# Kernel optimization log

Measured on AMD Instinct MI355X. Metric: run time of the kernel, lower is better.

Reference implementation:

```python
import jax, jax.numpy as jnp
import numpy as np

COS_EPS = 1e-6
LN_EPS = 1e-5

def _cosine_sim(a, b):
    # PyTorch F.cosine_similarity(dim=1, eps): dot / (max(||a||,eps)*max(||b||,eps))
    dot = jnp.sum(a * b, axis=1)
    na = jnp.maximum(jnp.linalg.norm(a, axis=1), COS_EPS)
    nb = jnp.maximum(jnp.linalg.norm(b, axis=1), COS_EPS)
    return dot / (na * nb)

def _layer_norm(x, gamma, beta):
    mu = jnp.mean(x, axis=-1, keepdims=True)
    var = jnp.mean(jnp.square(x - mu), axis=-1, keepdims=True)
    return (x - mu) * jax.lax.rsqrt(var + LN_EPS) * gamma + beta

def setup_inputs() -> dict:
    B, I, H = 8192, 1024, 1024
    key = jax.random.key(0)
    ks = jax.random.split(key, 10)
    s_in = 1.0 / np.sqrt(I + H)
    s_im = 1.0 / np.sqrt(I)
    return {
        "x": jax.random.normal(ks[0], (B, I), jnp.float32),
        "hx": jax.random.normal(ks[1], (B, H), jnp.float32),
        "cx": jax.random.normal(ks[2], (B, H), jnp.float32),
        # main gate linear: [I+H, 4H]
        "W": jax.random.uniform(ks[3], (I + H, 4 * H), jnp.float32, -s_in, s_in),
        "b": jax.random.uniform(ks[4], (4 * H,), jnp.float32, -s_in, s_in),
        # input_mapped: [I, H]
        "Wm": jax.random.uniform(ks[5], (I, H), jnp.float32, -s_im, s_im),
        "bm": jax.random.uniform(ks[6], (H,), jnp.float32, -s_im, s_im),
        # 4 LayerNorms (i, f, g, o)
        "gammas": 1.0 + 0.1 * jax.random.normal(ks[7], (4, H), jnp.float32),
        "betas": 0.1 * jax.random.normal(ks[8], (4, H), jnp.float32),
    }

def reference(x, hx, cx, W, b, Wm, bm, gammas, betas):
    H = hx.shape[1]
    # cosine attention gate between mapped input and hidden state
    input_mapped = x @ Wm + bm                                   # [B, H]
    attn = jax.nn.sigmoid(_cosine_sim(input_mapped, hx))[:, None]  # [B, 1]
    x_mod = x + attn * x
    gates = jnp.concatenate([x_mod, hx], axis=1) @ W + b         # [B, 4H]
    i_g, f_g, g_g, o_g = jnp.split(gates, 4, axis=1)
    i_g = jax.nn.sigmoid(_layer_norm(i_g, gammas[0], betas[0]))
    f_g = jax.nn.sigmoid(_layer_norm(f_g, gammas[1], betas[1]))
    g_g = jnp.tanh(_layer_norm(g_g, gammas[2], betas[2]))
    o_g = jax.nn.sigmoid(_layer_norm(o_g, gammas[3], betas[3]))
    cx_new = f_g * cx + i_g * g_g
    hx_new = o_g * jnp.tanh(cx_new)
    gate_co = jax.nn.sigmoid((_cosine_sim(hx_new, cx_new)[:, None] + 1.0) / 2.0)
    hx_modulated = hx_new + hx_new * gate_co
    return (hx_modulated, cx_new)
```

## Files before the change

kernel.cpp:

```cpp
#include <hip/hip_runtime.h>
#include <hip/hip_bf16.h>

#define DEV __device__ __forceinline__

typedef unsigned short u16;
typedef unsigned int u32;
typedef __attribute__((ext_vector_type(8))) short bf16x8;
typedef __attribute__((ext_vector_type(4))) float f32x4;

DEV float bf2f(u16 v) { u32 u = ((u32)v) << 16; return __builtin_bit_cast(float, u); }
DEV u16 f2bf(float f) {
    u32 u = __builtin_bit_cast(u32, f);
    u32 r = (u + 0x7fffu + ((u >> 16) & 1u)) >> 16;
    return (u16)r;
}
DEV float lo16(u32 u) { return __builtin_bit_cast(float, u << 16); }
DEV float hi16(u32 u) { return __builtin_bit_cast(float, u & 0xffff0000u); }
DEV float sigm(float x) { return 1.f / (1.f + __expf(-x)); }
DEV float clamp4(float v) { return fminf(fmaxf(v, -1e4f), 1e4f); }
DEV float loadf(const void* p, size_t i, int isf) {
    return isf ? clamp4(((const float*)p)[i]) : clamp4(bf2f(((const u16*)p)[i]));
}
DEV void load8(const void* p, size_t off, int isf, float* o) {
    if (isf) {
        const float* s = (const float*)p + off;
#pragma unroll
        for (int e = 0; e < 8; ++e) o[e] = clamp4(s[e]);
    } else {
        uint4 q = *(const uint4*)((const u16*)p + off);
        o[0] = clamp4(lo16(q.x)); o[1] = clamp4(hi16(q.x));
        o[2] = clamp4(lo16(q.y)); o[3] = clamp4(hi16(q.y));
        o[4] = clamp4(lo16(q.z)); o[5] = clamp4(hi16(q.z));
        o[6] = clamp4(lo16(q.w)); o[7] = clamp4(hi16(q.w));
    }
}
DEV uint4 pack8(const float* a) {
    uint4 q;
    q.x = (u32)f2bf(a[0]) | ((u32)f2bf(a[1]) << 16);
    q.y = (u32)f2bf(a[2]) | ((u32)f2bf(a[3]) << 16);
    q.z = (u32)f2bf(a[4]) | ((u32)f2bf(a[5]) << 16);
    q.w = (u32)f2bf(a[6]) | ((u32)f2bf(a[7]) << 16);
    return q;
}
DEV void store8(void* p, size_t off, int isf, const float* a) {
    if (isf) {
        float* d = (float*)p + off;
        *(float4*)(d) = (float4){a[0], a[1], a[2], a[3]};
        *(float4*)(d + 4) = (float4){a[4], a[5], a[6], a[7]};
    } else {
        *(uint4*)((u16*)p + off) = pack8(a);
    }
}

DEV void gload16(const void* g, void* l) {
    __builtin_amdgcn_global_load_lds(
        (const __attribute__((address_space(1))) void*)g,
        (__attribute__((address_space(3))) void*)l, 16, 0, 0);
}

__global__ void detect_dtype(const u32* __restrict__ xw, u32* __restrict__ flag) {
    const int lane = threadIdx.x & 63;
    int cnt = 0;
    for (int k = 0; k < 32; ++k) {
        u32 e = (xw[lane + 64 * k] >> 7) & 0xff;
        cnt += (e >= 118 && e <= 130) ? 1 : 0;
    }
#pragma unroll
    for (int off = 32; off > 0; off >>= 1) cnt += __shfl_xor(cnt, off, 64);
    if (lane == 0) *flag = (cnt > 1024) ? 0u : 1u;
}

__global__ __launch_bounds__(256) void cvt_bf16(const void* __restrict__ src,
                                                u16* __restrict__ dst, int n8,
                                                const u32* __restrict__ flagp) {
    const int isf = (int)*flagp;
    if (!isf) return;
    int i = blockIdx.x * 256 + threadIdx.x;
    if (i >= n8) return;
    size_t off = (size_t)i * 8;
    float a[8];
    load8(src, off, isf, a);
    *(uint4*)(dst + off) = pack8(a);
}

__global__ __launch_bounds__(256) void tr_any(const void* __restrict__ src,
                                              u16* __restrict__ dst,
                                              int R, int C,
                                              const u32* __restrict__ flagp) {
    const int isf = (int)*flagp;
    __shared__ __align__(16) u16 t[32][33];
    int tx = threadIdx.x & 31, ty = threadIdx.x >> 5;
    int c0 = blockIdx.x * 32, r0 = blockIdx.y * 32;
#pragma unroll
    for (int i = 0; i < 32; i += 8)
        t[ty + i][tx] = f2bf(loadf(src, (size_t)(r0 + ty + i) * C + (c0 + tx), isf));
    __syncthreads();
#pragma unroll
    for (int i = 0; i < 32; i += 8)
        dst[(size_t)(c0 + ty + i) * R + (r0 + tx)] = t[tx][ty + i];
}

__global__ __launch_bounds__(512, 2) void gemm256(
    const u16* __restrict__ A0c, const void* __restrict__ A0r,
    const u16* __restrict__ A1c, const void* __restrict__ A1r, int K0,
    const u16* __restrict__ Bt, const void* __restrict__ bias,
    const u32* __restrict__ flagp,
    u16* __restrict__ Cout, int M, int N, int K) {
    const int isf = (int)*flagp;
    const u16* const A0 = isf ? A0c : (const u16*)A0r;
    const u16* const A1 = isf ? A1c : (const u16*)A1r;
    __shared__ __align__(16) u16 lds[65536];
    u16* const ldsA = lds;
    u16* const ldsB = lds + 32768;
    const int tid = threadIdx.x;
    const int wave = tid >> 6, lane = tid & 63;
    const int wm = wave >> 2, wn = wave & 3;

    int bx = blockIdx.x, by = blockIdx.y;
    {
        const int gx = gridDim.x;
        const int nwg = gx * gridDim.y;
        if ((nwg & 7) == 0) {
            int lid = by * gx + bx;
            int swz = (lid & 7) * (nwg >> 3) + (lid >> 3);
            bx = swz % gx; by = swz / gx;
        }
    }
    const int m0 = by * 256, n0 = bx * 256;
    const int NT = K >> 6;

    size_t qA[2][2], qB[2][2];
#pragma unroll
    for (int h = 0; h < 2; ++h)
#pragma unroll
        for (int c = 0; c < 2; ++c) {
            int p = h * 16384 + c * 8192 + wave * 1024 + lane * 16;
            int lg = p ^ (((p >> 9) & 1) << 5);
            int s = lg >> 10, lr = (lg >> 6) & 15;
            int k = ((s & 1) << 5) + ((lg & 63) >> 1);
            int m = ((s >> 3) & 1) * 128 + ((s >> 4) & 1) * 64 +
                    ((s >> 1) & 3) * 16 + lr;
            qA[h][c] = (size_t)(m0 + m) * (size_t)K0 + (size_t)k;
            int ns = ((s >> 2) & 3) * 64 + ((s >> 4) & 1) * 32 +
                     ((s >> 1) & 1) * 16 + lr;
            int gn = (ns & ~63) | ((ns & 15) * 4 + ((ns >> 4) & 3));
            qB[h][c] = (size_t)(n0 + gn) * (size_t)K + (size_t)k;
        }

    const int mrow = lane & 15;
    const int kfr = (lane >> 4) * 8;
    const int aSwz = (mrow * 32 + kfr) ^ ((mrow & 8) << 1);

    f32x4 acc[8][4];
#pragma unroll
    for (int i = 0; i < 8; ++i)
#pragma unroll
        for (int j = 0; j < 4; ++j) acc[i][j] = (f32x4){0.f, 0.f, 0.f, 0.f};

#define ASEG(kt, AS_, KK_) const u16* AS_; int KK_; \
    if ((kt) < K0) { AS_ = A0; KK_ = (kt); } else { AS_ = A1; KK_ = (kt) - K0; }

    {
        ASEG(0, As0, kk0);
        gload16(As0 + qA[0][0] + kk0, ldsA + wave * 512);
        gload16(As0 + qA[0][1] + kk0, ldsA + 4096 + wave * 512);
        gload16(Bt + qB[1][0], ldsB + 8192 + wave * 512);
        gload16(Bt + qB[1][1], ldsB + 8192 + 4096 + wave * 512);
        gload16(As0 + qA[1][0] + kk0, ldsA + 8192 + wave * 512);
        gload16(As0 + qA[1][1] + kk0, ldsA + 8192 + 4096 + wave * 512);
        gload16(Bt + qB[0][0], ldsB + wave * 512);
        gload16(Bt + qB[0][1], ldsB + 4096 + wave * 512);
        if (NT > 1) {
            ASEG(64, As1, kk1);
            gload16(As1 + qA[0][0] + kk1, ldsA + 16384 + wave * 512);
            gload16(As1 + qA[0][1] + kk1, ldsA + 16384 + 4096 + wave * 512);
            gload16(Bt + qB[1][0] + 64, ldsB + 16384 + 8192 + wave * 512);
            gload16(Bt + qB[1][1] + 64, ldsB + 16384 + 8192 + 4096 + wave * 512);
            gload16(As1 + qA[1][0] + kk1, ldsA + 16384 + 8192 + wave * 512);
            gload16(As1 + qA[1][1] + kk1, ldsA + 16384 + 8192 + 4096 + wave * 512);
            asm volatile("s_waitcnt vmcnt(6)" ::: "memory");
        } else {
            asm volatile("s_waitcnt vmcnt(0)" ::: "memory");
        }
        __builtin_amdgcn_s_barrier();
    }

    for (int t = 0; t < NT; ++t) {
        const int bufb = (t & 1) << 14;
        const int obufb = bufb ^ 16384;
        const int k0 = t << 6;
        bf16x8 af0[4][2], af1[4][2], bfA[2][2], bfB[2][2];

        {
            const u16* ab = &ldsA[bufb + (wm * 8) * 512];
#pragma unroll
            for (int mt2 = 0; mt2 < 4; ++mt2)
#pragma unroll
                for (int ks = 0; ks < 2; ++ks)
                    af0[mt2][ks] = *(const bf16x8*)&ab[(mt2 * 2 + ks) * 512 + aSwz];
            const u16* bb = &ldsB[bufb + (wn * 4) * 512];
#pragma unroll
            for (int nt2 = 0; nt2 < 2; ++nt2)
#pragma unroll
                for (int ks = 0; ks < 2; ++ks)
                    bfA[nt2][ks] = *(const bf16x8*)&bb[(nt2 * 2 + ks) * 512 + aSwz];
        }
        if (t + 1 < NT) {
            gload16(Bt + qB[0][0] + (k0 + 64), ldsB + obufb + wave * 512);
            gload16(Bt + qB[0][1] + (k0 + 64), ldsB + obufb + 4096 + wave * 512);
        }
        __builtin_amdgcn_s_barrier();
        __builtin_amdgcn_s_setprio(1);
#pragma unroll
        for (int mt2 = 0; mt2 < 4; ++mt2)
#pragma unroll
            for (int nt2 = 0; nt2 < 2; ++nt2)
#pragma unroll
                for (int ks = 0; ks < 2; ++ks)
                    acc[mt2][nt2] = __builtin_amdgcn_mfma_f32_16x16x32_bf16(
                        af0[mt2][ks], bfA[nt2][ks], acc[mt2][nt2], 0, 0, 0);
        __builtin_amdgcn_s_setprio(0);

        {
            const u16* bb = &ldsB[bufb + (16 + wn * 4) * 512];
#pragma unroll
            for (int nt2 = 0; nt2 < 2; ++nt2)
#pragma unroll
                for (int ks = 0; ks < 2; ++ks)
                    bfB[nt2][ks] = *(const bf16x8*)&bb[(nt2 * 2 + ks) * 512 + aSwz];
        }
        __builtin_amdgcn_s_barrier();
        if (t + 2 < NT) {
            ASEG(k0 + 128, As2, kk2);
            gload16(As2 + qA[0][0] + kk2, ldsA + bufb + wave * 512);
            gload16(As2 + qA[0][1] + kk2, ldsA + bufb + 4096 + wave * 512);
        }
        __builtin_amdgcn_s_setprio(1);
#pragma unroll
        for (int mt2 = 0; mt2 < 4; ++mt2)
#pragma unroll
            for (int nt2 = 0; nt2 < 2; ++nt2)
#pragma unroll
                for (int ks = 0; ks < 2; ++ks)
                    acc[mt2][2 + nt2] = __builtin_amdgcn_mfma_f32_16x16x32_bf16(
                        af0[mt2][ks], bfB[nt2][ks], acc[mt2][2 + nt2], 0, 0, 0);
        __builtin_amdgcn_s_setprio(0);

        {
            const u16* ab = &ldsA[bufb + (16 + wm * 8) * 512];
#pragma unroll
            for (int mt2 = 0; mt2 < 4; ++mt2)
#pragma unroll
                for (int ks = 0; ks < 2; ++ks)
                    af1[mt2][ks] = *(const bf16x8*)&ab[(mt2 * 2 + ks) * 512 + aSwz];
        }
        __builtin_amdgcn_s_barrier();
        if (t + 2 < NT) {
            gload16(Bt + qB[1][0] + (k0 + 128), ldsB + bufb + 8192 + wave * 512);
            gload16(Bt + qB[1][1] + (k0 + 128), ldsB + bufb + 8192 + 4096 + wave * 512);
        }
        __builtin_amdgcn_s_setprio(1);
#pragma unroll
        for (int mt2 = 0; mt2 < 4; ++mt2)
#pragma unroll
            for (int nt2 = 0; nt2 < 2; ++nt2)
#pragma unroll
                for (int ks = 0; ks < 2; ++ks)
                    acc[4 + mt2][2 + nt2] = __builtin_amdgcn_mfma_f32_16x16x32_bf16(
                        af1[mt2][ks], bfB[nt2][ks], acc[4 + mt2][2 + nt2], 0, 0, 0);
        __builtin_amdgcn_s_setprio(0);

        __builtin_amdgcn_s_barrier();
        if (t + 2 < NT) {
            ASEG(k0 + 128, As3, kk3);
            gload16(As3 + qA[1][0] + kk3, ldsA + bufb + 8192 + wave * 512);
            gload16(As3 + qA[1][1] + kk3, ldsA + bufb + 8192 + 4096 + wave * 512);
        }
        __builtin_amdgcn_s_setprio(1);
#pragma unroll
        for (int mt2 = 0; mt2 < 4; ++mt2)
#pragma unroll
            for (int nt2 = 0; nt2 < 2; ++nt2)
#pragma unroll
                for (int ks = 0; ks < 2; ++ks)
                    acc[4 + mt2][nt2] = __builtin_amdgcn_mfma_f32_16x16x32_bf16(
                        af1[mt2][ks], bfA[nt2][ks], acc[4 + mt2][nt2], 0, 0, 0);
        __builtin_amdgcn_s_setprio(0);
        if (t + 2 < NT) {
            asm volatile("s_waitcnt vmcnt(6)" ::: "memory");
        } else {
            asm volatile("s_waitcnt vmcnt(0)" ::: "memory");
        }
        __builtin_amdgcn_s_barrier();
    }
#undef ASEG

    const int q = lane >> 4;
    const int cbase = n0 + wn * 64 + mrow * 4;
    float bv[4];
#pragma unroll
    for (int tt = 0; tt < 4; ++tt) bv[tt] = loadf(bias, cbase + tt, isf);
#pragma unroll
    for (int mt = 0; mt < 8; ++mt) {
        int row0 = m0 + wm * 128 + mt * 16 + q * 4;
#pragma unroll
        for (int r = 0; r < 4; ++r) {
            uint2 pk;
            pk.x = (u32)f2bf(acc[mt][0][r] + bv[0]) |
                   ((u32)f2bf(acc[mt][1][r] + bv[1]) << 16);
            pk.y = (u32)f2bf(acc[mt][2][r] + bv[2]) |
                   ((u32)f2bf(acc[mt][3][r] + bv[3]) << 16);
            *(uint2*)(Cout + (size_t)(row0 + r) * N + cbase) = pk;
        }
    }
}

__global__ __launch_bounds__(256) void attn_xmod(
    const u16* __restrict__ im,
    const u16* __restrict__ hxc, const void* __restrict__ hxr,
    const u16* __restrict__ xc, const void* __restrict__ xr,
    const u32* __restrict__ flagp, u16* __restrict__ xmod) {
    const int isf = (int)*flagp;
    const u16* hx = isf ? hxc : (const u16*)hxr;
    const u16* x = isf ? xc : (const u16*)xr;
    const int lane = threadIdx.x & 63;
    const int row = blockIdx.x * 4 + (threadIdx.x >> 6);
    float dot = 0.f, na = 0.f, nb = 0.f;
#pragma unroll
    for (int j = 0; j < 2; ++j) {
        size_t off = (size_t)row * 1024 + lane * 8 + j * 512;
        float a[8], h[8];
        load8(im, off, 0, a);
        load8(hx, off, 0, h);
#pragma unroll
        for (int e = 0; e < 8; ++e) {
            dot += a[e] * h[e]; na += a[e] * a[e]; nb += h[e] * h[e];
        }
    }
#pragma unroll
    for (int off = 32; off > 0; off >>= 1) {
        dot += __shfl_xor(dot, off, 64);
        na += __shfl_xor(na, off, 64);
        nb += __shfl_xor(nb, off, 64);
    }
    float cs = dot / (fmaxf(sqrtf(na), 1e-6f) * fmaxf(sqrtf(nb), 1e-6f));
    float fac = 1.f + sigm(cs);
#pragma unroll
    for (int j = 0; j < 2; ++j) {
        size_t off = (size_t)row * 1024 + lane * 8 + j * 512;
        float a[8];
        load8(x, off, 0, a);
#pragma unroll
        for (int e = 0; e < 8; ++e) a[e] *= fac;
        *(uint4*)(xmod + off) = pack8(a);
    }
}

__global__ __launch_bounds__(256) void ln_lstm(
    const u16* __restrict__ gates, const void* __restrict__ cx,
    const void* __restrict__ gammas, const void* __restrict__ betas,
    const u32* __restrict__ flagp, void* __restrict__ out, int BH) {
    const int isf = (int)*flagp;
    const int lane = threadIdx.x & 63;
    const int row = blockIdx.x * 4 + (threadIdx.x >> 6);
    float v[4][16];
    float s[4] = {0.f, 0.f, 0.f, 0.f}, ss[4] = {0.f, 0.f, 0.f, 0.f};
#pragma unroll
    for (int c = 0; c < 4; ++c) {
#pragma unroll
        for (int j = 0; j < 2; ++j) {
            size_t off = (size_t)row * 4096 + c * 1024 + lane * 8 + j * 512;
            float* vp = &v[c][j * 8];
            load8(gates, off, 0, vp);
#pragma unroll
            for (int e = 0; e < 8; ++e) { s[c] += vp[e]; ss[c] += vp[e] * vp[e]; }
        }
    }
#pragma unroll
    for (int off = 32; off > 0; off >>= 1) {
#pragma unroll
        for (int c = 0; c < 4; ++c) {
            s[c] += __shfl_xor(s[c], off, 64);
            ss[c] += __shfl_xor(ss[c], off, 64);
        }
    }
    float mean[4], rstd[4];
#pragma unroll
    for (int c = 0; c < 4; ++c) {
        mean[c] = s[c] * (1.f / 1024.f);
        float var = ss[c] * (1.f / 1024.f) - mean[c] * mean[c];
        rstd[c] = rsqrtf(fmaxf(var, 0.f) + 1e-5f);
    }
#pragma unroll
    for (int c = 0; c < 4; ++c) {
#pragma unroll
        for (int j = 0; j < 2; ++j) {
            size_t off = (size_t)(c * 1024 + lane * 8 + j * 512);
            float g[8], bb[8];
            load8(gammas, off, isf, g);
            load8(betas, off, isf, bb);
            float* vp = &v[c][j * 8];
#pragma unroll
            for (int e = 0; e < 8; ++e) {
                float y = (vp[e] - mean[c]) * rstd[c] * g[e] + bb[e];
                vp[e] = (c == 2) ? tanhf(y) : sigm(y);
            }
        }
    }
    float hn[16], cn[16];
    float dot = 0.f, nh = 0.f, nc = 0.f;
#pragma unroll
    for (int j = 0; j < 2; ++j) {
        size_t off = (size_t)row * 1024 + lane * 8 + j * 512;
        float cv[8];
        load8(cx, off, isf, cv);
#pragma unroll
        for (int e = 0; e < 8; ++e) {
            int idx = j * 8 + e;
            float c_new = v[1][idx] * cv[e] + v[0][idx] * v[2][idx];
            float h_new = v[3][idx] * tanhf(c_new);
            cn[idx] = c_new; hn[idx] = h_new;
            dot += h_new * c_new; nh += h_new * h_new; nc += c_new * c_new;
        }
    }
#pragma unroll
    for (int off = 32; off > 0; off >>= 1) {
        dot += __shfl_xor(dot, off, 64);
        nh += __shfl_xor(nh, off, 64);
        nc += __shfl_xor(nc, off, 64);
    }
    float cs = dot / (fmaxf(sqrtf(nh), 1e-6f) * fmaxf(sqrtf(nc), 1e-6f));
    float fac = 1.f + sigm((cs + 1.f) * 0.5f);
#pragma unroll
    for (int j = 0; j < 2; ++j) {
        size_t off = (size_t)row * 1024 + lane * 8 + j * 512;
        float ho[8];
#pragma unroll
        for (int e = 0; e < 8; ++e) ho[e] = hn[j * 8 + e] * fac;
        store8(out, off, isf, ho);
        store8(out, (size_t)BH + off, isf, &cn[j * 8]);
    }
}

__global__ void diag_k(u32* __restrict__ out, int ws_ok, int sizes_ok) {
    const int lane = threadIdx.x & 63;
    int mrow = lane & 15, quad = lane >> 4;
    bf16x8 af, bfr;
#pragma unroll
    for (int j = 0; j < 8; ++j) {
        int k = quad * 8 + j;
        af[j] = (short)f2bf((float)(((mrow * 7 + k * 3) % 11) - 5));
        bfr[j] = (short)f2bf((float)(((mrow * 5 + k * 2) % 13) - 6));
    }
    f32x4 cacc = (f32x4){0.f, 0.f, 0.f, 0.f};
    cacc = __builtin_amdgcn_mfma_f32_16x16x32_bf16(af, bfr, cacc, 0, 0, 0);
    int bad = 0;
#pragma unroll
    for (int r = 0; r < 4; ++r) {
        int mr = quad * 4 + r;
        float expv = 0.f;
        for (int k = 0; k < 32; ++k)
            expv += (float)(((mr * 7 + k * 3) % 11) - 5) *
                    (float)(((mrow * 5 + k * 2) % 13) - 6);
        if (fabsf(cacc[r] - expv) > 0.5f) bad = 1;
    }
    int mfma_bad = (__ballot(bad) != 0ull) ? 1 : 0;
    if (lane == 0) {
        if (!sizes_ok)     out[0] = __builtin_bit_cast(u32, 65536.f);
        else if (!ws_ok)   out[0] = __builtin_bit_cast(u32, 131072.f);
        else if (mfma_bad) out[0] = __builtin_bit_cast(u32, 32768.f);
    }
}

extern "C" void kernel_launch(void* const* d_in, const int* in_sizes, int n_in,
                              void* d_out, int out_size, void* d_ws, size_t ws_size,
                              hipStream_t stream) {
    const void* x   = d_in[0];
    const void* hx  = d_in[1];
    const void* cx  = d_in[2];
    const void* W   = d_in[3];
    const void* b   = d_in[4];
    const void* Wm  = d_in[5];
    const void* bm  = d_in[6];
    const void* gam = d_in[7];
    const void* bet = d_in[8];

    const int B = 8192, I = 1024, H = 1024;
    const int K2 = I + H, N2 = 4 * H;
    const size_t MiB = 1048576ull;

    char* ws = (char*)d_ws;
    u16* x_c   = (u16*)ws;
    u16* hx_c  = (u16*)(ws + 16 * MiB);
    u16* Wt    = (u16*)(ws + 32 * MiB);
    u16* Wmt   = (u16*)(ws + 48 * MiB);
    u16* gates = (u16*)(ws + 50 * MiB);
    u32* flag  = (u32*)(ws + 114 * MiB);
    u16* xmod  = (u16*)d_out;
    u16* imb   = (u16*)d_out + 8388608ull;

    const int sizes_ok =
        n_in == 9 && out_size == 16777216 &&
        in_sizes[0] == 8388608 && in_sizes[1] == 8388608 && in_sizes[2] == 8388608 &&
        in_sizes[3] == 8388608 && in_sizes[4] == 4096 && in_sizes[5] == 1048576 &&
        in_sizes[6] == 1024 && in_sizes[7] == 4096 && in_sizes[8] == 4096;
    const int ws_ok = ws_size >= 115 * MiB;

    if (sizes_ok && ws_ok) {
        detect_dtype<<<1, 64, 0, stream>>>((const u32*)x, flag);
        cvt_bf16<<<4096, 256, 0, stream>>>(x, x_c, 1048576, flag);
        cvt_bf16<<<4096, 256, 0, stream>>>(hx, hx_c, 1048576, flag);
        tr_any<<<dim3(H / 32, I / 32), 256, 0, stream>>>(Wm, Wmt, I, H, flag);
        tr_any<<<dim3(N2 / 32, K2 / 32), 256, 0, stream>>>(W, Wt, K2, N2, flag);
        gemm256<<<dim3(H / 256, B / 256), 512, 0, stream>>>(
            x_c, x, x_c, x, I, Wmt, bm, flag, imb, B, H, I);
        attn_xmod<<<dim3(B / 4), 256, 0, stream>>>(imb, hx_c, hx, x_c, x, flag, xmod);
        gemm256<<<dim3(N2 / 256, B / 256), 512, 0, stream>>>(
            xmod, xmod, hx_c, hx, I, Wt, b, flag, gates, B, N2, K2);
        ln_lstm<<<dim3(B / 4), 256, 0, stream>>>(gates, cx, gam, bet, flag,
                                                 d_out, B * H);
    }
    diag_k<<<1, 64, 0, stream>>>((u32*)d_out, ws_ok, sizes_ok);
}
```

Measured before the change: 412.1 us.

## Reorder GEMM main loop to prefetch next-tile fragments and merge conversion kernels

```diff
diff --git a/kernel.cpp b/kernel.cpp
--- a/kernel.cpp
+++ b/kernel.cpp
@@ -70,17 +70,20 @@
     if (lane == 0) *flag = (cnt > 1024) ? 0u : 1u;
 }
 
-__global__ __launch_bounds__(256) void cvt_bf16(const void* __restrict__ src,
-                                                u16* __restrict__ dst, int n8,
-                                                const u32* __restrict__ flagp) {
+__global__ __launch_bounds__(256) void cvt2_bf16(
+    const void* __restrict__ sa, const void* __restrict__ sb,
+    u16* __restrict__ da, u16* __restrict__ db, int n8each,
+    const u32* __restrict__ flagp) {
     const int isf = (int)*flagp;
     if (!isf) return;
     int i = blockIdx.x * 256 + threadIdx.x;
-    if (i >= n8) return;
-    size_t off = (size_t)i * 8;
+    const void* s; u16* d; int j;
+    if (i < n8each) { s = sa; d = da; j = i; }
+    else            { s = sb; d = db; j = i - n8each; }
+    size_t off = (size_t)j * 8;
     float a[8];
-    load8(src, off, isf, a);
-    *(uint4*)(dst + off) = pack8(a);
+    load8(s, off, 1, a);
+    *(uint4*)(d + off) = pack8(a);
 }
 
 __global__ __launch_bounds__(256) void tr_any(const void* __restrict__ src,
@@ -185,25 +188,34 @@
         __builtin_amdgcn_s_barrier();
     }
 
+    bf16x8 af0[4][2], af1[4][2], bfA[2][2], bfB[2][2];
+    {
+        const u16* ab = &ldsA[(wm * 8) * 512];
+#pragma unroll
+        for (int mt2 = 0; mt2 < 4; ++mt2)
+#pragma unroll
+            for (int ks = 0; ks < 2; ++ks)
+                af0[mt2][ks] = *(const bf16x8*)&ab[(mt2 * 2 + ks) * 512 + aSwz];
+        const u16* bb = &ldsB[(wn * 4) * 512];
+#pragma unroll
+        for (int nt2 = 0; nt2 < 2; ++nt2)
+#pragma unroll
+            for (int ks = 0; ks < 2; ++ks)
+                bfA[nt2][ks] = *(const bf16x8*)&bb[(nt2 * 2 + ks) * 512 + aSwz];
+    }
+
     for (int t = 0; t < NT; ++t) {
         const int bufb = (t & 1) << 14;
         const int obufb = bufb ^ 16384;
         const int k0 = t << 6;
-        bf16x8 af0[4][2], af1[4][2], bfA[2][2], bfB[2][2];
 
         {
-            const u16* ab = &ldsA[bufb + (wm * 8) * 512];
+            const u16* ab = &ldsA[bufb + (16 + wm * 8) * 512];
 #pragma unroll
             for (int mt2 = 0; mt2 < 4; ++mt2)
 #pragma unroll
                 for (int ks = 0; ks < 2; ++ks)
-                    af0[mt2][ks] = *(const bf16x8*)&ab[(mt2 * 2 + ks) * 512 + aSwz];
-            const u16* bb = &ldsB[bufb + (wn * 4) * 512];
-#pragma unroll
-            for (int nt2 = 0; nt2 < 2; ++nt2)
-#pragma unroll
-                for (int ks = 0; ks < 2; ++ks)
-                    bfA[nt2][ks] = *(const bf16x8*)&bb[(nt2 * 2 + ks) * 512 + aSwz];
+                    af1[mt2][ks] = *(const bf16x8*)&ab[(mt2 * 2 + ks) * 512 + aSwz];
         }
         if (t + 1 < NT) {
             gload16(Bt + qB[0][0] + (k0 + 64), ldsB + obufb + wave * 512);
@@ -242,22 +254,43 @@
             for (int nt2 = 0; nt2 < 2; ++nt2)
 #pragma unroll
                 for (int ks = 0; ks < 2; ++ks)
+                    acc[4 + mt2][nt2] = __builtin_amdgcn_mfma_f32_16x16x32_bf16(
+                        af1[mt2][ks], bfA[nt2][ks], acc[4 + mt2][nt2], 0, 0, 0);
+#pragma unroll
+        for (int mt2 = 0; mt2 < 4; ++mt2)
+#pragma unroll
+            for (int nt2 = 0; nt2 < 2; ++nt2)
+#pragma unroll
+                for (int ks = 0; ks < 2; ++ks)
                     acc[mt2][2 + nt2] = __builtin_amdgcn_mfma_f32_16x16x32_bf16(
                         af0[mt2][ks], bfB[nt2][ks], acc[mt2][2 + nt2], 0, 0, 0);
         __builtin_amdgcn_s_setprio(0);
 
-        {
-            const u16* ab = &ldsA[bufb + (16 + wm * 8) * 512];
-#pragma unroll
-            for (int mt2 = 0; mt2 < 4; ++mt2)
-#pragma unroll
-                for (int ks = 0; ks < 2; ++ks)
-                    af1[mt2][ks] = *(const bf16x8*)&ab[(mt2 * 2 + ks) * 512 + aSwz];
-        }
         __builtin_amdgcn_s_barrier();
         if (t + 2 < NT) {
             gload16(Bt + qB[1][0] + (k0 + 128), ldsB + bufb + 8192 + wave * 512);
             gload16(Bt + qB[1][1] + (k0 + 128), ldsB + bufb + 8192 + 4096 + wave * 512);
+            ASEG(k0 + 128, As3, kk3);
+            gload16(As3 + qA[1][0] + kk3, ldsA + bufb + 8192 + wave * 512);
+            gload16(As3 + qA[1][1] + kk3, ldsA + bufb + 8192 + 4096 + wave * 512);
+            asm volatile("s_waitcnt vmcnt(6)" ::: "memory");
+        } else {
+            asm volatile("s_waitcnt vmcnt(0)" ::: "memory");
+        }
+        __builtin_amdgcn_s_barrier();
+        if (t + 1 < NT) {
+            const u16* ab = &ldsA[obufb + (wm * 8) * 512];
+#pragma unroll
+            for (int mt2 = 0; mt2 < 4; ++mt2)
+#pragma unroll
+                for (int ks = 0; ks < 2; ++ks)
+                    af0[mt2][ks] = *(const bf16x8*)&ab[(mt2 * 2 + ks) * 512 + aSwz];
+            const u16* bb = &ldsB[obufb + (wn * 4) * 512];
+#pragma unroll
+            for (int nt2 = 0; nt2 < 2; ++nt2)
+#pragma unroll
+                for (int ks = 0; ks < 2; ++ks)
+                    bfA[nt2][ks] = *(const bf16x8*)&bb[(nt2 * 2 + ks) * 512 + aSwz];
         }
         __builtin_amdgcn_s_setprio(1);
 #pragma unroll
@@ -269,29 +302,6 @@
                     acc[4 + mt2][2 + nt2] = __builtin_amdgcn_mfma_f32_16x16x32_bf16(
                         af1[mt2][ks], bfB[nt2][ks], acc[4 + mt2][2 + nt2], 0, 0, 0);
         __builtin_amdgcn_s_setprio(0);
-
-        __builtin_amdgcn_s_barrier();
-        if (t + 2 < NT) {
-            ASEG(k0 + 128, As3, kk3);
-            gload16(As3 + qA[1][0] + kk3, ldsA + bufb + 8192 + wave * 512);
-            gload16(As3 + qA[1][1] + kk3, ldsA + bufb + 8192 + 4096 + wave * 512);
-        }
-        __builtin_amdgcn_s_setprio(1);
-#pragma unroll
-        for (int mt2 = 0; mt2 < 4; ++mt2)
-#pragma unroll
-            for (int nt2 = 0; nt2 < 2; ++nt2)
-#pragma unroll
-                for (int ks = 0; ks < 2; ++ks)
-                    acc[4 + mt2][nt2] = __builtin_amdgcn_mfma_f32_16x16x32_bf16(
-                        af1[mt2][ks], bfA[nt2][ks], acc[4 + mt2][nt2], 0, 0, 0);
-        __builtin_amdgcn_s_setprio(0);
-        if (t + 2 < NT) {
-            asm volatile("s_waitcnt vmcnt(6)" ::: "memory");
-        } else {
-            asm volatile("s_waitcnt vmcnt(0)" ::: "memory");
-        }
-        __builtin_amdgcn_s_barrier();
     }
 #undef ASEG
 
@@ -508,8 +518,7 @@
 
     if (sizes_ok && ws_ok) {
         detect_dtype<<<1, 64, 0, stream>>>((const u32*)x, flag);
-        cvt_bf16<<<4096, 256, 0, stream>>>(x, x_c, 1048576, flag);
-        cvt_bf16<<<4096, 256, 0, stream>>>(hx, hx_c, 1048576, flag);
+        cvt2_bf16<<<8192, 256, 0, stream>>>(x, hx, x_c, hx_c, 1048576, flag);
         tr_any<<<dim3(H / 32, I / 32), 256, 0, stream>>>(Wm, Wmt, I, H, flag);
         tr_any<<<dim3(N2 / 32, K2 / 32), 256, 0, stream>>>(W, Wt, K2, N2, flag);
         gemm256<<<dim3(H / 256, B / 256), 512, 0, stream>>>(
```

Result: no change. 411.3 us (-0.2%).
